# Kernel optimization log

Measured on AMD Instinct MI355X. Metric: run time of the kernel, lower is better.

Reference implementation:

```python
import jax, jax.numpy as jnp
import numpy as np

N_HEAD = 16

def setup_inputs() -> dict:
    key = jax.random.key(0)
    k1, k2, k3 = jax.random.split(key, 3)
    B, T, C = 4, 2048, 1024
    x = jax.random.normal(k1, (B, T, C), dtype=jnp.float32)
    W_attn = jax.random.normal(k2, (C, 3 * C), dtype=jnp.float32) * (1.0 / np.sqrt(C))
    b_attn = jnp.zeros((3 * C,), dtype=jnp.float32)
    W_proj = jax.random.normal(k3, (C, C), dtype=jnp.float32) * (1.0 / np.sqrt(C))
    b_proj = jnp.zeros((C,), dtype=jnp.float32)
    return {"x": x, "W_attn": W_attn, "b_attn": b_attn, "W_proj": W_proj, "b_proj": b_proj, "train": 0}

def reference(x, W_attn, b_attn, W_proj, b_proj, train):
    # Causal self-attention, eval mode (dropout = identity since dropout=0.0 / train=False).
    B, T, C = x.shape
    H = N_HEAD
    hd = C // H
    qkv = x @ W_attn + b_attn                      # [B, T, 3C]
    q, k, v = jnp.split(qkv, 3, axis=-1)
    def to_heads(a):
        return a.reshape(B, T, H, hd).swapaxes(1, 2)   # [B, H, T, hd]
    q, k, v = to_heads(q), to_heads(k), to_heads(v)
    scale = 1.0 / jnp.sqrt(jnp.asarray(hd, dtype=x.dtype))
    attn = jnp.einsum('bhqd,bhkd->bhqk', q, k) * scale   # [B, H, T, T]
    causal = jnp.tril(jnp.ones((T, T), dtype=bool))
    attn = jnp.where(causal, attn, -jnp.inf)
    p = jax.nn.softmax(attn, axis=-1)
    y = jnp.einsum('bhqk,bhkd->bhqd', p, v)              # [B, H, T, hd]
    y = y.swapaxes(1, 2).reshape(B, T, C)
    return y @ W_proj + b_proj
```

## Files before the change

kernel.cpp:

```cpp
#include <hip/hip_runtime.h>
#include <hip/hip_bf16.h>
#include <math.h>

typedef __attribute__((ext_vector_type(8))) short short8;
typedef __attribute__((ext_vector_type(4))) short short4v;
typedef __attribute__((ext_vector_type(4))) float floatx4;
using bf16 = __hip_bfloat16;

#define DEVI __device__ __forceinline__

DEVI floatx4 fzero4() { floatx4 z; z[0]=0.f; z[1]=0.f; z[2]=0.f; z[3]=0.f; return z; }

DEVI float ex2(float x) {
  float r;
  asm("v_exp_f32 %0, %1" : "=v"(r) : "v"(x));
  return r;
}

DEVI float max3f(float a, float b, float c) {
  float d;
  asm("v_max3_f32 %0, %1, %2, %3" : "=v"(d) : "v"(a), "v"(b), "v"(c));
  return d;
}

DEVI unsigned short f2b(float x) {
  union { bf16 h; unsigned short u; } c;
  c.h = __float2bfloat16(x);
  return c.u;
}

DEVI floatx4 mfma16(short4v a, short4v b, floatx4 c) {
#if __has_builtin(__builtin_amdgcn_mfma_f32_16x16x16bf16_1k)
  return __builtin_amdgcn_mfma_f32_16x16x16bf16_1k(a, b, c, 0, 0, 0);
#else
  floatx4 d;
  asm("v_mfma_f32_16x16x16_bf16 %0, %1, %2, %3" : "=v"(d) : "v"(a), "v"(b), "v"(c));
  return d;
#endif
}

DEVI void gload16(const bf16* g, bf16* l) {
  typedef __attribute__((address_space(1))) const void gv_t;
  typedef __attribute__((address_space(3))) void lv_t;
  __builtin_amdgcn_global_load_lds((gv_t*)g, (lv_t*)l, 16, 0, 0);
}

__global__ __launch_bounds__(256) void k_cast(const float* __restrict__ in,
                                              bf16* __restrict__ out, int n) {
  int i = (blockIdx.x * 256 + threadIdx.x) * 8;
  if (i >= n) return;
  float4 a = *(const float4*)(in + i);
  float4 b = *(const float4*)(in + i + 4);
  short8 v;
  v[0] = (short)f2b(a.x); v[1] = (short)f2b(a.y);
  v[2] = (short)f2b(a.z); v[3] = (short)f2b(a.w);
  v[4] = (short)f2b(b.x); v[5] = (short)f2b(b.y);
  v[6] = (short)f2b(b.z); v[7] = (short)f2b(b.w);
  *(short8*)(out + i) = v;
}

__global__ __launch_bounds__(256) void k_transpose(const float* __restrict__ in,
                                                   bf16* __restrict__ out,
                                                   int R, int C) {
  __shared__ float tile[32][33];
  int x = blockIdx.x * 32 + threadIdx.x;
  for (int i = threadIdx.y; i < 32; i += 8) {
    int y = blockIdx.y * 32 + i;
    tile[i][threadIdx.x] = (y < R && x < C) ? in[(size_t)y * C + x] : 0.f;
  }
  __syncthreads();
  int ox = blockIdx.y * 32 + threadIdx.x;
  for (int i = threadIdx.y; i < 32; i += 8) {
    int oy = blockIdx.x * 32 + i;
    if (oy < C && ox < R) out[(size_t)oy * R + ox] = __float2bfloat16(tile[threadIdx.x][i]);
  }
}

template<int MODE>
__global__ __launch_bounds__(256) void k_gemm(
    const bf16* __restrict__ A, const bf16* __restrict__ Bt,
    const float* __restrict__ bias,
    bf16* __restrict__ Qo, bf16* __restrict__ Ko, bf16* __restrict__ Vo,
    float* __restrict__ Fo, int M, int N, int Kd) {
  __shared__ bf16 sA[2][128 * 32];
  __shared__ bf16 sB[2][128 * 32];
  const int tid = threadIdx.x;
  const int w = tid >> 6, l = tid & 63;
  const int lg = l >> 4, li = l & 15;
  const int wr = w >> 1, wc = w & 1;
  const int ii = blockIdx.x >> 3, xcd = blockIdx.x & 7;
  const int bx = ii >> 3, by = xcd * 8 + (ii & 7);
  const int m0 = by * 128, n0 = bx * 128;

  const int r0 = tid >> 2, ko0 = (tid & 3) * 8;
  const bf16* pa0 = A + (size_t)(m0 + r0) * Kd + ko0;
  const bf16* pa1 = A + (size_t)(m0 + 64 + r0) * Kd + ko0;
  const bf16* pb0 = Bt + (size_t)(n0 + r0) * Kd + ko0;
  const bf16* pb1 = Bt + (size_t)(n0 + 64 + r0) * Kd + ko0;

  floatx4 acc[4][4];
#pragma unroll
  for (int i = 0; i < 4; ++i)
#pragma unroll
    for (int j = 0; j < 4; ++j) acc[i][j] = fzero4();

  auto STAGE = [&](int buf, int k0) {
    gload16(pa0 + k0, &sA[buf][w * 512]);
    gload16(pa1 + k0, &sA[buf][2048 + w * 512]);
    gload16(pb0 + k0, &sB[buf][w * 512]);
    gload16(pb1 + k0, &sB[buf][2048 + w * 512]);
  };

  STAGE(0, 0);
  int cur = 0;
  for (int k0 = 0; k0 < Kd; k0 += 32) {
    if (k0 + 32 < Kd) {
      STAGE(cur ^ 1, k0 + 32);
      asm volatile("s_waitcnt vmcnt(4)" ::: "memory");
    } else {
      asm volatile("s_waitcnt vmcnt(0)" ::: "memory");
    }
    __builtin_amdgcn_s_barrier();
    short8 af[4], bfr[4];
#pragma unroll
    for (int i = 0; i < 4; ++i)
      af[i] = *(const short8*)&sA[cur][(wr * 64 + i * 16 + li) * 32 + lg * 8];
#pragma unroll
    for (int j = 0; j < 4; ++j)
      bfr[j] = *(const short8*)&sB[cur][(wc * 64 + j * 16 + li) * 32 + lg * 8];
#pragma unroll
    for (int i = 0; i < 4; ++i)
#pragma unroll
      for (int j = 0; j < 4; ++j)
        acc[i][j] = __builtin_amdgcn_mfma_f32_16x16x32_bf16(af[i], bfr[j], acc[i][j], 0, 0, 0);
    __builtin_amdgcn_s_barrier();
    cur ^= 1;
  }

#pragma unroll
  for (int i = 0; i < 4; ++i) {
#pragma unroll
    for (int j = 0; j < 4; ++j) {
      const int ng = n0 + wc * 64 + j * 16 + li;
      const float bs = bias[ng];
      const int mgb = m0 + wr * 64 + i * 16 + lg * 4;
      if (MODE == 0) {
        const int bb = mgb >> 11, t = mgb & 2047;
        const int d = ng & 63;
        if (ng < 1024) {
          const int h = ng >> 6;
#pragma unroll
          for (int r = 0; r < 4; ++r)
            Qo[(((size_t)bb * 16 + h) * 2048 + t + r) * 64 + d] =
                __float2bfloat16((acc[i][j][r] + bs) * 0.18033688011112042f);
        } else if (ng < 2048) {
          const int h = (ng - 1024) >> 6;
#pragma unroll
          for (int r = 0; r < 4; ++r)
            Ko[(((size_t)bb * 16 + h) * 2048 + t + r) * 64 + d] =
                __float2bfloat16(acc[i][j][r] + bs);
        } else {
          const int h = (ng - 2048) >> 6;
          short4v vv;
#pragma unroll
          for (int r = 0; r < 4; ++r) vv[r] = (short)f2b(acc[i][j][r] + bs);
          *(short4v*)&Vo[(((size_t)bb * 16 + h) * 64 + d) * 2048 + t] = vv;
        }
      } else {
#pragma unroll
        for (int r = 0; r < 4; ++r)
          Fo[(size_t)(mgb + r) * N + ng] = acc[i][j][r] + bs;
      }
    }
  }
}

#define T_SEQ 2048

__global__ __launch_bounds__(256) void k_attn(
    const bf16* __restrict__ Q, const bf16* __restrict__ K,
    const bf16* __restrict__ Vt, bf16* __restrict__ Y) {
  __shared__ bf16 sK[2][64 * 64];
  __shared__ bf16 sV[2][64 * 64];

  const int tid = threadIdx.x;
  const int w = tid >> 6, l = tid & 63;
  const int lg = l >> 4, li = l & 15;
  const int bid = blockIdx.x;
  const int sq = bid >> 3;
  const int bh = (bid & 7) * 8 + (sq & 7);
  const int g = sq >> 3;
  const int qd = g >> 2, rr = g & 3;
  const int tb = (qd == 0) ? 15 - rr : (qd == 1) ? 8 + rr : (qd == 2) ? 7 - rr : rr;
  const int b = bh >> 4, h = bh & 15;

  const bf16* Qp = Q + (size_t)bh * (T_SEQ * 64);
  const bf16* Kp = K + (size_t)bh * (T_SEQ * 64);
  const bf16* Vp = Vt + (size_t)bh * (64 * T_SEQ);

  const int q0 = tb * 128;
  const int wq0 = q0 + w * 32;
  const int nst = (q0 + 128) >> 6;

  short8 aq[2][2];
#pragma unroll
  for (int rg = 0; rg < 2; ++rg)
#pragma unroll
    for (int dc = 0; dc < 2; ++dc)
      aq[rg][dc] = *(const short8*)(Qp + (size_t)(wq0 + rg * 16 + li) * 64 + dc * 32 + lg * 8);

  floatx4 o[2][4];
#pragma unroll
  for (int rg = 0; rg < 2; ++rg)
#pragma unroll
    for (int f = 0; f < 4; ++f) o[rg][f] = fzero4();
  float m[2] = {-INFINITY, -INFINITY};
  float lsum[2] = {0.f, 0.f};

  auto STAGE = [&](int buf, int k0) {
#pragma unroll
    for (int half = 0; half < 2; ++half) {
      const int c = half * 256 + tid;
      const int row = c >> 3, cs = c & 7;
      const int sc = cs ^ (row & 7);
      bf16* kb = &sK[buf][(half * 256 + w * 64) * 8];
      bf16* vb = &sV[buf][(half * 256 + w * 64) * 8];
      gload16(Kp + (size_t)(k0 + row) * 64 + sc * 8, kb);
      gload16(Vp + (size_t)row * T_SEQ + k0 + sc * 8, vb);
    }
  };

  int cur = 0;
  STAGE(0, 0);
  for (int t = 0; t < nst; ++t) {
    const int k0 = t << 6;
    if (t + 1 < nst) {
      STAGE(cur ^ 1, k0 + 64);
      asm volatile("s_waitcnt vmcnt(4)" ::: "memory");
    } else {
      asm volatile("s_waitcnt vmcnt(0)" ::: "memory");
    }
    __builtin_amdgcn_s_barrier();
    if (k0 <= wq0 + 31) {
      floatx4 s[2][4];
      __builtin_amdgcn_s_setprio(1);
#pragma unroll
      for (int kt = 0; kt < 4; ++kt) {
        const int rowk = kt * 16 + li;
        const short8 kb0 = *(const short8*)&sK[cur][rowk * 64 + ((lg ^ (rowk & 7)) * 8)];
        const short8 kb1 = *(const short8*)&sK[cur][rowk * 64 + (((4 + lg) ^ (rowk & 7)) * 8)];
#pragma unroll
        for (int rg = 0; rg < 2; ++rg) {
          floatx4 acc = __builtin_amdgcn_mfma_f32_16x16x32_bf16(kb0, aq[rg][0], fzero4(), 0, 0, 0);
          s[rg][kt] = __builtin_amdgcn_mfma_f32_16x16x32_bf16(kb1, aq[rg][1], acc, 0, 0, 0);
        }
      }
      __builtin_amdgcn_s_setprio(0);
      if (k0 + 63 > wq0) {
#pragma unroll
        for (int rg = 0; rg < 2; ++rg) {
          const int qg = wq0 + rg * 16 + li;
#pragma unroll
          for (int kt = 0; kt < 4; ++kt) {
            const int kgb = k0 + kt * 16 + lg * 4;
#pragma unroll
            for (int r = 0; r < 4; ++r)
              if (kgb + r > qg) s[rg][kt][r] = -1e30f;
          }
        }
      }
      float pm[2];
#pragma unroll
      for (int rg = 0; rg < 2; ++rg) {
        float t0 = max3f(s[rg][0][0], s[rg][0][1], s[rg][0][2]);
        float t1 = max3f(s[rg][0][3], s[rg][1][0], s[rg][1][1]);
        float t2 = max3f(s[rg][1][2], s[rg][1][3], s[rg][2][0]);
        float t3 = max3f(s[rg][2][1], s[rg][2][2], s[rg][2][3]);
        float t4 = max3f(s[rg][3][0], s[rg][3][1], s[rg][3][2]);
        float p = fmaxf(max3f(t0, t1, t2), max3f(t3, t4, s[rg][3][3]));
        p = fmaxf(p, __shfl_xor(p, 16));
        p = fmaxf(p, __shfl_xor(p, 32));
        pm[rg] = p;
      }
      const float need = fmaxf(pm[0] - m[0], pm[1] - m[1]);
      if (!__all(need <= 8.0f)) {
#pragma unroll
        for (int rg = 0; rg < 2; ++rg) {
          const float mn = fmaxf(m[rg], pm[rg]);
          const float a = ex2(m[rg] - mn);
          m[rg] = mn;
          lsum[rg] *= a;
          float ar[4];
#pragma unroll
          for (int r = 0; r < 4; ++r) ar[r] = __shfl(a, lg * 4 + r);
#pragma unroll
          for (int f = 0; f < 4; ++f) {
            o[rg][f][0] *= ar[0]; o[rg][f][1] *= ar[1];
            o[rg][f][2] *= ar[2]; o[rg][f][3] *= ar[3];
          }
        }
      }
      short4v pa4[2][4];
#pragma unroll
      for (int rg = 0; rg < 2; ++rg) {
#pragma unroll
        for (int kt = 0; kt < 4; ++kt) {
          const float e0 = ex2(s[rg][kt][0] - m[rg]);
          const float e1 = ex2(s[rg][kt][1] - m[rg]);
          const float e2 = ex2(s[rg][kt][2] - m[rg]);
          const float e3 = ex2(s[rg][kt][3] - m[rg]);
          lsum[rg] += (e0 + e1) + (e2 + e3);
          short4v pv;
          pv[0] = (short)f2b(e0); pv[1] = (short)f2b(e1);
          pv[2] = (short)f2b(e2); pv[3] = (short)f2b(e3);
          pa4[rg][kt] = pv;
        }
      }
      __builtin_amdgcn_s_setprio(1);
#pragma unroll
      for (int f = 0; f < 4; ++f) {
        const int rowv = f * 16 + li;
        const int rx = rowv & 7;
#pragma unroll
        for (int kt = 0; kt < 4; ++kt) {
          const int cc = 2 * kt + (lg >> 1);
          const short4v vb4 = *(const short4v*)&sV[cur][rowv * 64 + (((cc ^ rx) << 3) | ((lg & 1) << 2))];
          o[0][f] = mfma16(pa4[0][kt], vb4, o[0][f]);
          o[1][f] = mfma16(pa4[1][kt], vb4, o[1][f]);
        }
      }
      __builtin_amdgcn_s_setprio(0);
    }
    __builtin_amdgcn_s_barrier();
    cur ^= 1;
  }
#pragma unroll
  for (int rg = 0; rg < 2; ++rg) {
    float Ls = lsum[rg];
    Ls += __shfl_xor(Ls, 16);
    Ls += __shfl_xor(Ls, 32);
#pragma unroll
    for (int r = 0; r < 4; ++r) {
      const float inv = 1.0f / __shfl(Ls, lg * 4 + r);
      const int qg = wq0 + rg * 16 + lg * 4 + r;
      const size_t base = ((size_t)b * T_SEQ + qg) * 1024 + h * 64;
#pragma unroll
      for (int f = 0; f < 4; ++f)
        Y[base + f * 16 + li] = __float2bfloat16(o[rg][f][r] * inv);
    }
  }
}

extern "C" void kernel_launch(void* const* d_in, const int* in_sizes, int n_in,
                              void* d_out, int out_size, void* d_ws, size_t ws_size,
                              hipStream_t stream) {
  const float* x      = (const float*)d_in[0];
  const float* W_attn = (const float*)d_in[1];
  const float* b_attn = (const float*)d_in[2];
  const float* W_proj = (const float*)d_in[3];
  const float* b_proj = (const float*)d_in[4];
  float* out = (float*)d_out;

  char* ws = (char*)d_ws;
  bf16* Wt_a = (bf16*)(ws);
  bf16* Wt_p = (bf16*)(ws + 6291456);
  bf16* Qb   = (bf16*)(ws + 8388608);
  bf16* Kb   = (bf16*)(ws + 25165824);
  bf16* Vtb  = (bf16*)(ws + 41943040);
  bf16* x_bf = (bf16*)(ws + 58720256);
  bf16* Yb   = x_bf;

  k_cast<<<4096, 256, 0, stream>>>(x, x_bf, 8388608);
  k_transpose<<<dim3(96, 32), dim3(32, 8), 0, stream>>>(W_attn, Wt_a, 1024, 3072);
  k_transpose<<<dim3(32, 32), dim3(32, 8), 0, stream>>>(W_proj, Wt_p, 1024, 1024);
  k_gemm<0><<<1536, 256, 0, stream>>>(x_bf, Wt_a, b_attn, Qb, Kb, Vtb,
                                      nullptr, 8192, 3072, 1024);
  k_attn<<<1024, 256, 0, stream>>>(Qb, Kb, Vtb, Yb);
  k_gemm<1><<<512, 256, 0, stream>>>(Yb, Wt_p, b_proj, nullptr, nullptr,
                                     nullptr, out, 8192, 1024, 1024);
}
```

Measured before the change: 189.5 us.

## Use 256x256-tile 512-thread GEMM with swizzled async loads for QKV projection

Replaces the QKV projection GEMM (128x128 tiles, 256 threads) with a dedicated kernel that uses 256x256 output tiles, 8 waves, BK=64, and XOR-swizzled LDS layout. Global-to-LDS loads go through gload16 and are staged in four phases interleaved with MFMA work using explicit vmcnt waits and setprio. The goal is more data reuse per byte loaded and better overlap of loads with compute. The cost is higher register pressure from 32 accumulators per wave and only 384 blocks, so fewer blocks per CU and a coarser wave schedule.

```diff
diff --git a/kernel.cpp b/kernel.cpp
--- a/kernel.cpp
+++ b/kernel.cpp
@@ -76,12 +76,137 @@
   }
 }
 
-template<int MODE>
+#define LOG2E_O8 0.18033688011112042f
+
+__global__ __launch_bounds__(512) void k_gemm8(
+    const bf16* __restrict__ A, const bf16* __restrict__ Bt,
+    const float* __restrict__ bias,
+    bf16* __restrict__ Qo, bf16* __restrict__ Ko, bf16* __restrict__ Vo) {
+  __shared__ bf16 sA[2][16384];
+  __shared__ bf16 sB[2][16384];
+  const int Kd = 1024;
+  const int tid = threadIdx.x;
+  const int w = tid >> 6, l = tid & 63;
+  const int lg = l >> 4, li = l & 15;
+  const int ii = blockIdx.x >> 3, xcd = blockIdx.x & 7;
+  const int by = xcd * 4 + (ii & 3), bx = ii >> 2;
+  const int m0 = by * 256, n0 = bx * 256;
+
+  const int arow = tid >> 3;
+  const int acs = (tid & 7) ^ (arow & 7);
+  const int swz = (li & 7);
+
+  auto STAGE_A = [&](int buf, int k0, int q) {
+    gload16(A + (size_t)(m0 + q * 64 + arow) * Kd + k0 + acs * 8,
+            &sA[buf][q * 4096 + w * 512]);
+  };
+  auto STAGE_B = [&](int buf, int k0, int h) {
+    gload16(Bt + (size_t)(n0 + h * 128 + arow) * Kd + k0 + acs * 8,
+            &sB[buf][h * 8192 + w * 512]);
+    gload16(Bt + (size_t)(n0 + h * 128 + 64 + arow) * Kd + k0 + acs * 8,
+            &sB[buf][h * 8192 + 4096 + w * 512]);
+  };
+
+  floatx4 acc[16][2];
+#pragma unroll
+  for (int i = 0; i < 16; ++i) { acc[i][0] = fzero4(); acc[i][1] = fzero4(); }
+  short8 bfr[2][2];
+
+  STAGE_B(0, 0, 0); STAGE_B(0, 0, 1);
+  STAGE_A(0, 0, 0); STAGE_A(0, 0, 1); STAGE_A(0, 0, 2); STAGE_A(0, 0, 3);
+
+#define GPHASE(P)                                                               \
+  {                                                                             \
+    if (pf) {                                                                   \
+      if (P == 0) STAGE_B(nxt, k1, 0);                                          \
+      if (P == 1) STAGE_B(nxt, k1, 1);                                          \
+      if (P == 2) { STAGE_A(nxt, k1, 0); STAGE_A(nxt, k1, 1); }                 \
+      if (P == 3) { STAGE_A(nxt, k1, 2); STAGE_A(nxt, k1, 3); }                 \
+      asm volatile("s_waitcnt vmcnt(4)" ::: "memory");                          \
+    } else {                                                                    \
+      asm volatile("s_waitcnt vmcnt(0)" ::: "memory");                          \
+    }                                                                           \
+    __builtin_amdgcn_s_barrier();                                               \
+    if (P == 0) {                                                               \
+      _Pragma("unroll")                                                         \
+      for (int j = 0; j < 2; ++j) {                                             \
+        const int rb = w * 32 + j * 16 + li;                                    \
+        const int h = rb >> 7, rl = rb & 127;                                   \
+        _Pragma("unroll")                                                       \
+        for (int kc = 0; kc < 2; ++kc)                                          \
+          bfr[j][kc] = *(const short8*)&sB[cur][h * 8192 + rl * 64 +            \
+                                               (((kc * 4 + lg) ^ swz) * 8)];    \
+      }                                                                         \
+    }                                                                           \
+    short8 af[4][2];                                                            \
+    _Pragma("unroll")                                                           \
+    for (int i2 = 0; i2 < 4; ++i2)                                              \
+      _Pragma("unroll")                                                         \
+      for (int kc = 0; kc < 2; ++kc)                                            \
+        af[i2][kc] = *(const short8*)&sA[cur][P * 4096 + (i2 * 16 + li) * 64 +  \
+                                              (((kc * 4 + lg) ^ swz) * 8)];     \
+    __builtin_amdgcn_s_setprio(1);                                              \
+    _Pragma("unroll")                                                           \
+    for (int i2 = 0; i2 < 4; ++i2)                                              \
+      _Pragma("unroll")                                                         \
+      for (int j = 0; j < 2; ++j) {                                             \
+        acc[P * 4 + i2][j] = __builtin_amdgcn_mfma_f32_16x16x32_bf16(           \
+            af[i2][0], bfr[j][0], acc[P * 4 + i2][j], 0, 0, 0);                 \
+        acc[P * 4 + i2][j] = __builtin_amdgcn_mfma_f32_16x16x32_bf16(           \
+            af[i2][1], bfr[j][1], acc[P * 4 + i2][j], 0, 0, 0);                 \
+      }                                                                         \
+    __builtin_amdgcn_s_setprio(0);                                              \
+    __builtin_amdgcn_s_barrier();                                               \
+  }
+
+  int cur = 0;
+  for (int T = 0; T < 16; ++T) {
+    const int k1 = (T + 1) << 6;
+    const int nxt = cur ^ 1;
+    const bool pf = (T + 1 < 16);
+    GPHASE(0)
+    GPHASE(1)
+    GPHASE(2)
+    GPHASE(3)
+    cur = nxt;
+  }
+#undef GPHASE
+
+#pragma unroll
+  for (int i = 0; i < 16; ++i) {
+#pragma unroll
+    for (int j = 0; j < 2; ++j) {
+      const int ng = n0 + w * 32 + j * 16 + li;
+      const float bs = bias[ng];
+      const int mgb = m0 + i * 16 + lg * 4;
+      const int bb = mgb >> 11, t = mgb & 2047;
+      const int d = ng & 63;
+      if (ng < 1024) {
+        const int h = ng >> 6;
+#pragma unroll
+        for (int r = 0; r < 4; ++r)
+          Qo[(((size_t)bb * 16 + h) * 2048 + t + r) * 64 + d] =
+              __float2bfloat16((acc[i][j][r] + bs) * LOG2E_O8);
+      } else if (ng < 2048) {
+        const int h = (ng - 1024) >> 6;
+#pragma unroll
+        for (int r = 0; r < 4; ++r)
+          Ko[(((size_t)bb * 16 + h) * 2048 + t + r) * 64 + d] =
+              __float2bfloat16(acc[i][j][r] + bs);
+      } else {
+        const int h = (ng - 2048) >> 6;
+        short4v vv;
+#pragma unroll
+        for (int r = 0; r < 4; ++r) vv[r] = (short)f2b(acc[i][j][r] + bs);
+        *(short4v*)&Vo[(((size_t)bb * 16 + h) * 64 + d) * 2048 + t] = vv;
+      }
+    }
+  }
+}
+
 __global__ __launch_bounds__(256) void k_gemm(
     const bf16* __restrict__ A, const bf16* __restrict__ Bt,
-    const float* __restrict__ bias,
-    bf16* __restrict__ Qo, bf16* __restrict__ Ko, bf16* __restrict__ Vo,
-    float* __restrict__ Fo, int M, int N, int Kd) {
+    const float* __restrict__ bias, float* __restrict__ Fo, int N, int Kd) {
   __shared__ bf16 sA[2][128 * 32];
   __shared__ bf16 sB[2][128 * 32];
   const int tid = threadIdx.x;
@@ -144,33 +269,9 @@
       const int ng = n0 + wc * 64 + j * 16 + li;
       const float bs = bias[ng];
       const int mgb = m0 + wr * 64 + i * 16 + lg * 4;
-      if (MODE == 0) {
-        const int bb = mgb >> 11, t = mgb & 2047;
-        const int d = ng & 63;
-        if (ng < 1024) {
-          const int h = ng >> 6;
-#pragma unroll
-          for (int r = 0; r < 4; ++r)
-            Qo[(((size_t)bb * 16 + h) * 2048 + t + r) * 64 + d] =
-                __float2bfloat16((acc[i][j][r] + bs) * 0.18033688011112042f);
-        } else if (ng < 2048) {
-          const int h = (ng - 1024) >> 6;
-#pragma unroll
-          for (int r = 0; r < 4; ++r)
-            Ko[(((size_t)bb * 16 + h) * 2048 + t + r) * 64 + d] =
-                __float2bfloat16(acc[i][j][r] + bs);
-        } else {
-          const int h = (ng - 2048) >> 6;
-          short4v vv;
-#pragma unroll
-          for (int r = 0; r < 4; ++r) vv[r] = (short)f2b(acc[i][j][r] + bs);
-          *(short4v*)&Vo[(((size_t)bb * 16 + h) * 64 + d) * 2048 + t] = vv;
-        }
-      } else {
-#pragma unroll
-        for (int r = 0; r < 4; ++r)
-          Fo[(size_t)(mgb + r) * N + ng] = acc[i][j][r] + bs;
-      }
+#pragma unroll
+      for (int r = 0; r < 4; ++r)
+        Fo[(size_t)(mgb + r) * N + ng] = acc[i][j][r] + bs;
     }
   }
 }
@@ -373,9 +474,7 @@
   k_cast<<<4096, 256, 0, stream>>>(x, x_bf, 8388608);
   k_transpose<<<dim3(96, 32), dim3(32, 8), 0, stream>>>(W_attn, Wt_a, 1024, 3072);
   k_transpose<<<dim3(32, 32), dim3(32, 8), 0, stream>>>(W_proj, Wt_p, 1024, 1024);
-  k_gemm<0><<<1536, 256, 0, stream>>>(x_bf, Wt_a, b_attn, Qb, Kb, Vtb,
-                                      nullptr, 8192, 3072, 1024);
+  k_gemm8<<<384, 512, 0, stream>>>(x_bf, Wt_a, b_attn, Qb, Kb, Vtb);
   k_attn<<<1024, 256, 0, stream>>>(Qb, Kb, Vtb, Yb);
-  k_gemm<1><<<512, 256, 0, stream>>>(Yb, Wt_p, b_proj, nullptr, nullptr,
-                                     nullptr, out, 8192, 1024, 1024);
-}
+  k_gemm<<<512, 256, 0, stream>>>(Yb, Wt_p, b_proj, out, 1024, 1024);
+}
```

Result: slower. 227.5 us (+20.0%).
